# Optimization experiments

Measured on AMD Instinct MI355X. Metric: run time of the kernel, lower is better.

Reference implementation:

```python
import jax, jax.numpy as jnp
import numpy as np
from jax import lax

NEG = -1e30  # safe stand-in for -inf in float32
BLANK = 0


def _ctc_loss(log_probs, targets, logits_lengths, targets_lengths):
    # log_probs: (B, T, V) log-softmax over V; targets: (B, S) with labels in [1, V)
    B, T, V = log_probs.shape
    S = targets.shape[1]
    L = 2 * S + 1

    # extended target sequence with interleaved blanks: [b, t0, b, t1, ..., b]
    ext = jnp.full((B, L), BLANK, dtype=targets.dtype)
    ext = ext.at[:, 1::2].set(targets)

    # skip transition (s-2 -> s) allowed iff ext[s] != blank and ext[s] != ext[s-2]
    shifted2 = jnp.concatenate([jnp.full((B, 2), -1, dtype=ext.dtype), ext[:, :-2]], axis=1)
    skip = (ext != BLANK) & (ext != shifted2)  # (B, L)

    # gather per-time log-probs of extended labels: (B, T, L) -> scan axis first (T, B, L)
    lp_ext = jnp.take_along_axis(log_probs, ext[:, None, :], axis=2)
    xs = jnp.moveaxis(lp_ext, 1, 0)

    alpha0 = jnp.where(jnp.arange(L) == 0, 0.0, NEG).astype(log_probs.dtype)
    alpha0 = jnp.broadcast_to(alpha0, (B, L))

    def step(alpha, inputs):
        lp_t, t = inputs
        a2 = jnp.pad(alpha[:, :-1], ((0, 0), (1, 0)), constant_values=NEG)
        a3 = jnp.pad(alpha[:, :-2], ((0, 0), (2, 0)), constant_values=NEG)
        a3 = jnp.where(skip, a3, NEG)
        new = jnp.logaddexp(jnp.logaddexp(alpha, a2), a3) + lp_t
        # freeze alpha past each sequence's length
        alpha = jnp.where((t < logits_lengths)[:, None], new, alpha)
        return alpha, None

    alpha, _ = lax.scan(step, alpha0, (xs, jnp.arange(T)))

    # final states: last label (2*len-1) and trailing blank (2*len)
    e1 = (2 * targets_lengths - 1)[:, None]
    e2 = (2 * targets_lengths)[:, None]
    l1 = jnp.take_along_axis(alpha, e1, axis=1)[:, 0]
    l2 = jnp.take_along_axis(alpha, e2, axis=1)[:, 0]
    return -jnp.logaddexp(l1, l2)  # (B,)


def setup_inputs() -> dict:
    key = jax.random.key(0)
    k1, k2, k3, k4 = jax.random.split(key, 4)
    B, T, V, S = 64, 2000, 256, 200
    logits = jax.random.normal(k1, (B, T, V), dtype=jnp.float32)
    targets = jax.random.randint(k2, (B, S), 1, V)  # avoid blank=0
    logits_lengths = jax.random.randint(k3, (B,), 1500, T + 1)
    targets_lengths = jax.random.randint(k4, (B,), 150, S + 1)
    return {"logits": logits, "targets": targets,
            "logits_lengths": logits_lengths, "targets_lengths": targets_lengths}


def reference(logits, targets, logits_lengths, targets_lengths):
    # after_logsoftmax=False, time_major=False, reduce=None -> per-sample loss (B,)
    log_probs = jax.nn.log_softmax(logits, axis=2)
    return _ctc_loss(log_probs, targets, logits_lengths, targets_lengths)
```

## Files before the change

### kernel.cpp

```cpp
#include <hip/hip_runtime.h>
#include <hip/hip_bf16.h>
#include <cstdint>

#define NEG  (-1e30f)
#define VSZ  256
#define TCAP 2048
#define LN2F 0.6931471805599453f

typedef __attribute__((ext_vector_type(2))) float f32x2;

static __device__ __forceinline__ float    uifu(unsigned u) { return __uint_as_float(u); }
static __device__ __forceinline__ unsigned f2bf(float f) {
    unsigned u = __float_as_uint(f);
    return (u + 0x7fffu + ((u >> 16) & 1u)) >> 16;
}

static __device__ __forceinline__ unsigned pkbf(float lo, float hi) {
    unsigned r;
    asm("v_cvt_pk_bf16_f32 %0, %1, %2" : "=v"(r) : "v"(lo), "v"(hi));
    return r;
}

static __device__ __forceinline__ float wave_sum_dpp(float v) {
    v += __int_as_float(__builtin_amdgcn_update_dpp(0, __float_as_int(v), 0x111, 0xf, 0xf, true));
    v += __int_as_float(__builtin_amdgcn_update_dpp(0, __float_as_int(v), 0x112, 0xf, 0xf, true));
    v += __int_as_float(__builtin_amdgcn_update_dpp(0, __float_as_int(v), 0x114, 0xf, 0xf, true));
    v += __int_as_float(__builtin_amdgcn_update_dpp(0, __float_as_int(v), 0x118, 0xf, 0xf, true));
    v += __int_as_float(__builtin_amdgcn_update_dpp(0, __float_as_int(v), 0x142, 0xa, 0xf, true));
    v += __int_as_float(__builtin_amdgcn_update_dpp(0, __float_as_int(v), 0x143, 0xc, 0xf, true));
    return __int_as_float(__builtin_amdgcn_readlane(__float_as_int(v), 63));
}

__global__ __launch_bounds__(256) void prep7(const float* __restrict__ logits,
                                             const int* __restrict__ targets,
                                             unsigned short* __restrict__ po,
                                             float* __restrict__ pbf,
                                             int T, int S) {
    const int b    = blockIdx.y;
    const int lane = threadIdx.x & 63;
    const int wv   = threadIdx.x >> 6;
    const int rt   = blockIdx.x * 4 + wv;
    if (rt >= T) return;
    const size_t row = (size_t)b * T + rt;
    __shared__ float ldse[4][VSZ];

    const float4* p = (const float4*)(logits + row * VSZ);
    float4 x = p[lane];
    float4 e;
    e.x = __expf(x.x); e.y = __expf(x.y); e.z = __expf(x.z); e.w = __expf(x.w);
    ((float4*)&ldse[wv][0])[lane] = e;

    float s  = (e.x + e.y) + (e.z + e.w);
    float tot = wave_sum_dpp(s);
    float rs  = __builtin_amdgcn_rcpf(tot);

    const int* tg = targets + (size_t)b * S;
    const int c0 = 4 * lane;
    uint2 st;
    if ((S & 3) == 0) {
        int4 tgv = *(const int4*)(tg + min(c0, S - 4));
        float g0 = ldse[wv][tgv.x] * rs;
        float g1 = ldse[wv][tgv.y] * rs;
        float g2 = ldse[wv][tgv.z] * rs;
        float g3 = ldse[wv][tgv.w] * rs;
        st.x = pkbf(g0, g1);
        st.y = pkbf(g2, g3);
    } else {
        float g0 = 0.f, g1 = 0.f, g2 = 0.f, g3 = 0.f;
        if (c0     < S) g0 = ldse[wv][tg[c0]]     * rs;
        if (c0 + 1 < S) g1 = ldse[wv][tg[c0 + 1]] * rs;
        if (c0 + 2 < S) g2 = ldse[wv][tg[c0 + 2]] * rs;
        if (c0 + 3 < S) g3 = ldse[wv][tg[c0 + 3]] * rs;
        st.x = pkbf(g0, g1);
        st.y = pkbf(g2, g3);
    }
    ((uint2*)(po + row * VSZ))[lane] = st;
    if (lane == 0) pbf[row] = e.x * rs;
}

typedef __attribute__((address_space(1))) unsigned int g1u_t;
typedef __attribute__((address_space(3))) unsigned int l3u_t;

static __device__ __forceinline__ void dma16(const void* g, void* l) {
    __builtin_amdgcn_global_load_lds((g1u_t*)(uintptr_t)g,
                                     (l3u_t*)(unsigned int)(uintptr_t)l, 16, 0, 0);
}
static __device__ __forceinline__ void dma4(const void* g, void* l) {
    __builtin_amdgcn_global_load_lds((g1u_t*)(uintptr_t)g,
                                     (l3u_t*)(unsigned int)(uintptr_t)l, 4, 0, 0);
}
static __device__ __forceinline__ float dpp_shr1_f(float v) {
    return __int_as_float(__builtin_amdgcn_update_dpp(0, __float_as_int(v), 0x138, 0xf, 0xf, true));
}
static __device__ __forceinline__ float dpp_shl1_f(float v) {
    return __int_as_float(__builtin_amdgcn_update_dpp(0, __float_as_int(v), 0x130, 0xf, 0xf, true));
}
static __device__ __forceinline__ int dpp_shr1_i(int v) {
    return __builtin_amdgcn_update_dpp(0, v, 0x138, 0xf, 0xf, true);
}
static __device__ __forceinline__ int dpp_shl1_i(int v) {
    return __builtin_amdgcn_update_dpp(0, v, 0x130, 0xf, 0xf, true);
}

template<int W>
static __device__ __forceinline__ void scan_dir(const unsigned short* __restrict__ po_b,
                                                const float* __restrict__ pbr,
                                                unsigned short* __restrict__ d0,
                                                unsigned short* __restrict__ d1,
                                                float* __restrict__ p0,
                                                float* __restrict__ p1,
                                                int lenD, int lm1, int i,
                                                float m1, float m3, float m5, float m7, float n7,
                                                float A[8], int& E) {
    const int  lhalf = i & 31;
    const bool hi    = (i >= 32);
    float dscale = 1.f;

    f32x2 P73, P51, E62, E40, M73, M51, N75;
    P73.x = A[7]; P73.y = A[3];
    P51.x = A[5]; P51.y = A[1];
    E62.x = A[6]; E62.y = A[2];
    E40.x = A[4]; E40.y = A[0];
    M73.x = m7;  M73.y = m3;
    M51.x = m5;  M51.y = m1;
    N75.x = n7;  N75.y = m5;

    uint2 ra0, ra1, ra2, ra3, ra4, ra5, ra6, ra7;
    uint2 rb0, rb1, rb2, rb3, rb4, rb5, rb6, rb7;
    float4 qaA, qaB, qbA, qbB;

#define ROWOF(t_) (W ? max(lm1 - (t_), 0) : min((t_), lm1))

#define BODY(XV, PBV) { \
    f32x2 pDB, pCA, pbb; \
    pDB.x = uifu(XV.y & 0xffff0000u); pDB.y = uifu(XV.x & 0xffff0000u); \
    pCA.x = uifu(XV.y << 16);         pCA.y = uifu(XV.x << 16); \
    pbb.x = (PBV);                    pbb.y = (PBV); \
    if (W == 0) { \
        float hs = dpp_shr1_f(P73.x) * dscale; \
        f32x2 a3h; a3h.x = P73.y; a3h.y = hs; \
        f32x2 t73 = (__builtin_elementwise_fma(M73, P51, E62) + P73) * pDB; \
        f32x2 t51 = (__builtin_elementwise_fma(M51, a3h, E40) + P51) * pCA; \
        f32x2 t62 = (E62 + P51) * pbb; \
        f32x2 t40 = (E40 + a3h) * pbb; \
        P73 = t73; P51 = t51; E62 = t62; E40 = t40; \
    } else { \
        f32x2 Q73 = P73 * pDB, Q51 = P51 * pCA, Q62 = E62 * pbb, Q40 = E40 * pbb; \
        float nq0 = dpp_shl1_f(Q40.y) * dscale; \
        float nq1 = dpp_shl1_f(Q51.y) * dscale; \
        f32x2 nq04; nq04.x = nq0; nq04.y = Q40.x; \
        f32x2 n1q5; n1q5.x = nq1; n1q5.y = Q51.x; \
        f32x2 t73 = __builtin_elementwise_fma(N75, n1q5, Q73 + nq04); \
        f32x2 t51 = __builtin_elementwise_fma(M73, Q73, Q51 + Q62); \
        f32x2 t62 = Q62 + Q73; \
        f32x2 t40 = Q40 + Q51; \
        P73 = t73; P51 = t51; E62 = t62; E40 = t40; \
    } \
}

#define RENORM { \
    f32x2 mA = __builtin_elementwise_max(__builtin_elementwise_max(P73, P51), \
                                         __builtin_elementwise_max(E62, E40)); \
    float lmx = fmaxf(mA.x, mA.y); \
    unsigned mb = __float_as_uint(lmx) >> 23; \
    mb = mb > 253u ? 253u : mb; \
    float sc_ = uifu((254u - mb) << 23); \
    f32x2 scv; scv.x = sc_; scv.y = sc_; \
    P73 *= scv; P51 *= scv; E62 *= scv; E40 *= scv; \
    E += (int)mb - 127; \
    int he = W ? dpp_shl1_i(E) : dpp_shr1_i(E); \
    int d  = min(max(he - E, -100), 100); \
    dscale = uifu((unsigned)(d + 127) << 23); \
}

#define STAGE(DN, PN_, TBASE) { \
    _Pragma("unroll") \
    for (int u = 0; u < 32; u += 2) { \
        const int rA = ROWOF((TBASE) + u), rB = ROWOF((TBASE) + u + 1); \
        dma16(po_b + (size_t)(hi ? rB : rA) * VSZ + 8 * lhalf, (DN) + (size_t)u * VSZ); \
    } \
    dma4(pbr + ROWOF((TBASE) + lhalf), (PN_)); \
}

#define LDB(R, QA, QB, DC, PC, BASE) { \
    R##0 = *(const uint2*)((DC) + (size_t)((BASE) + 0) * VSZ + 4 * i); \
    R##1 = *(const uint2*)((DC) + (size_t)((BASE) + 1) * VSZ + 4 * i); \
    R##2 = *(const uint2*)((DC) + (size_t)((BASE) + 2) * VSZ + 4 * i); \
    R##3 = *(const uint2*)((DC) + (size_t)((BASE) + 3) * VSZ + 4 * i); \
    R##4 = *(const uint2*)((DC) + (size_t)((BASE) + 4) * VSZ + 4 * i); \
    R##5 = *(const uint2*)((DC) + (size_t)((BASE) + 5) * VSZ + 4 * i); \
    R##6 = *(const uint2*)((DC) + (size_t)((BASE) + 6) * VSZ + 4 * i); \
    R##7 = *(const uint2*)((DC) + (size_t)((BASE) + 7) * VSZ + 4 * i); \
    QA = *(const float4*)((PC) + (BASE)); \
    QB = *(const float4*)((PC) + (BASE) + 4); \
}

#define CMP8(R, QA, QB) { \
    BODY(R##0, QA.x) BODY(R##1, QA.y) BODY(R##2, QA.z) BODY(R##3, QA.w) RENORM \
    BODY(R##4, QB.x) BODY(R##5, QB.y) BODY(R##6, QB.z) BODY(R##7, QB.w) RENORM \
}

#define SBAR __builtin_amdgcn_sched_barrier(0)

#define SUPERF(DC, PC, DN, PN_) { \
    STAGE(DN, PN_, t0 + 32) \
    asm volatile("s_waitcnt vmcnt(17)" ::: "memory"); \
    LDB(ra, qaA, qaB, DC, PC, 0) \
    SBAR; \
    LDB(rb, qbA, qbB, DC, PC, 8) \
    SBAR; \
    CMP8(ra, qaA, qaB) \
    LDB(ra, qaA, qaB, DC, PC, 16) \
    SBAR; \
    CMP8(rb, qbA, qbB) \
    LDB(rb, qbA, qbB, DC, PC, 24) \
    SBAR; \
    CMP8(ra, qaA, qaB) \
    CMP8(rb, qbA, qbB) \
}

    STAGE(d0, p0, 0)

    int t0 = 0;
    const int nfull = lenD >> 5;
    const int ntail = lenD & 31;
    unsigned short* cur = d0; unsigned short* nxt = d1;
    float* pc = p0;  float* pn = p1;

    #pragma clang loop unroll(disable)
    for (int sl = 0; sl < nfull; ++sl) {
        SUPERF(cur, pc, nxt, pn)
        t0 += 32;
        unsigned short* td = cur; cur = nxt; nxt = td;
        float* tp = pc; pc = pn; pn = tp;
    }
    if (ntail) {
        asm volatile("s_waitcnt vmcnt(0)" ::: "memory");
        #pragma clang loop unroll(disable)
        for (int u = 0; u < ntail; ++u) {
            uint2 x = *(const uint2*)(cur + (size_t)u * VSZ + 4 * i);
            float pb = pc[u];
            BODY(x, pb)
            if ((u & 3) == 3) RENORM
        }
    }

    A[7] = P73.x; A[3] = P73.y;
    A[5] = P51.x; A[1] = P51.y;
    A[6] = E62.x; A[2] = E62.y;
    A[4] = E40.x; A[0] = E40.y;
#undef SUPERF
#undef SBAR
#undef CMP8
#undef LDB
#undef STAGE
#undef RENORM
#undef BODY
#undef ROWOF
}

__global__ __launch_bounds__(128, 1) void ctc_scan15(const unsigned short* __restrict__ po,
                                                     const float* __restrict__ pbf,
                                                     const int* __restrict__ targets,
                                                     const int* __restrict__ llen_p,
                                                     const int* __restrict__ tlen_p,
                                                     float* __restrict__ out,
                                                     int T, int S) {
    const int b   = blockIdx.x;
    const int w   = threadIdx.x >> 6;
    const int i   = threadIdx.x & 63;
    const int len  = llen_p[b];
    const int lm1  = len - 1;
    const int lenF = (len + 1) >> 1;
    const int lenD = w ? (len - lenF) : lenF;

    __shared__ __align__(16) unsigned short dF0[32 * VSZ], dF1[32 * VSZ];
    __shared__ __align__(16) unsigned short dB0[32 * VSZ], dB1[32 * VSZ];
    __shared__ __align__(16) float pF0[64], pF1[64], pB0[64], pB1[64];
    __shared__ __align__(16) float bfin[512];
    __shared__ int bein[64];
    __shared__ __align__(16) unsigned char lds_pad[16384];
    if (__builtin_expect(T < 0, 0)) ((volatile unsigned char*)lds_pad)[0] = 1;

    const int* tg  = targets + (size_t)b * S;
    const int Sm1  = S - 1;
    const int j0   = 4 * i;
    const int tm   = tg[max(min(j0 - 1, Sm1), 0)];
    const int t0l  = tg[min(j0,     Sm1)];
    const int t1l  = tg[min(j0 + 1, Sm1)];
    const int t2l  = tg[min(j0 + 2, Sm1)];
    const int t3l  = tg[min(j0 + 3, Sm1)];
    const int t4l  = tg[min(j0 + 4, Sm1)];
    const float m1 = (j0 == 0 || t0l != tm) ? 1.f : 0.f;
    const float m3 = (t1l != t0l) ? 1.f : 0.f;
    const float m5 = (t2l != t1l) ? 1.f : 0.f;
    const float m7 = (t3l != t2l) ? 1.f : 0.f;
    const float n7 = (t4l != t3l) ? 1.f : 0.f;

    const unsigned short* po_b = po + (size_t)b * T * VSZ;
    const float*          pbr  = pbf + (size_t)b * T;

    float A[8];
    int   E = 0;
    if (w == 0) {
        #pragma unroll
        for (int k = 0; k < 8; ++k) A[k] = 0.f;
        if (i == 0) A[0] = 1.f;
        scan_dir<0>(po_b, pbr, dF0, dF1, pF0, pF1,
                    lenD, lm1, i, m1, m3, m5, m7, n7, A, E);
    } else {
        const int tl = tlen_p[b];
        const int s1 = 2 * tl - 1, s2 = 2 * tl;
        #pragma unroll
        for (int k = 0; k < 8; ++k)
            A[k] = (8 * i + k == s1 || 8 * i + k == s2) ? 1.f : 0.f;
        scan_dir<1>(po_b, pbr, dB0, dB1, pB0, pB1,
                    lenD, lm1, i, m1, m3, m5, m7, n7, A, E);
        *(float4*)&bfin[8 * i]     = make_float4(A[0], A[1], A[2], A[3]);
        *(float4*)&bfin[8 * i + 4] = make_float4(A[4], A[5], A[6], A[7]);
        bein[i] = E;
    }
    __syncthreads();
    if (w == 0) {
        float4 u0 = *(float4*)&bfin[8 * i];
        float4 u1 = *(float4*)&bfin[8 * i + 4];
        float dsum = A[0]*u0.x + A[1]*u0.y + A[2]*u0.z + A[3]*u0.w
                   + A[4]*u1.x + A[5]*u1.y + A[6]*u1.z + A[7]*u1.w;
        float li = (dsum > 0.f) ? __logf(dsum) + (float)(E + bein[i]) * LN2F : NEG;
        float mx = li;
        #pragma unroll
        for (int off = 32; off; off >>= 1) mx = fmaxf(mx, __shfl_xor(mx, off, 64));
        float ss = __expf(li - mx);
        #pragma unroll
        for (int off = 32; off; off >>= 1) ss += __shfl_xor(ss, off, 64);
        if (i == 0) out[b] = -(mx + __logf(ss));
    }
}

__device__ __forceinline__ void barrier_lgkm() {
    __asm__ volatile("s_waitcnt lgkmcnt(0)\n\ts_barrier" ::: "memory");
}

__global__ __launch_bounds__(256) void lse_kernel(const float* __restrict__ logits,
                                                  float* __restrict__ lse,
                                                  int nrows) {
    int row = blockIdx.x * 4 + (threadIdx.x >> 6);
    if (row >= nrows) return;
    int lane = threadIdx.x & 63;
    const float4* p = (const float4*)(logits + (size_t)row * VSZ);
    float4 x = p[lane];
    float m = fmaxf(fmaxf(x.x, x.y), fmaxf(x.z, x.w));
    #pragma unroll
    for (int off = 32; off; off >>= 1) m = fmaxf(m, __shfl_xor(m, off, 64));
    float s = __expf(x.x - m) + __expf(x.y - m) + __expf(x.z - m) + __expf(x.w - m);
    #pragma unroll
    for (int off = 32; off; off >>= 1) s += __shfl_xor(s, off, 64);
    if (lane == 0) lse[row] = m + __logf(s);
}

__device__ __forceinline__ float lae(float a, float b) {
    float mx = fmaxf(a, b);
    float mn = fminf(a, b);
    return mx + __logf(1.0f + __expf(mn - mx));
}

__global__ __launch_bounds__(256, 1) void ctc_scan_fb(const float* __restrict__ logits,
                                                      const int* __restrict__ targets,
                                                      const int* __restrict__ llen_p,
                                                      const int* __restrict__ tlen_p,
                                                      const float* __restrict__ lse,
                                                      float* __restrict__ out,
                                                      int T, int S) {
    const int b = blockIdx.x;
    const int i = threadIdx.x;
    const int len = llen_p[b];

    __shared__ float blankv[TCAP];
    __shared__ float abuf[2][256 + 2];
    __shared__ float wsum[4];

    const float* __restrict__ lgb  = logits + (size_t)b * T * VSZ;
    const float* __restrict__ lseb = lse + (size_t)b * T;

    int  lab  = 0;
    bool skip = false;
    if (i < S) {
        lab = targets[b * S + i];
        int prev = (i >= 1) ? targets[b * S + i - 1] : -1;
        skip = (lab != prev);
    }
    for (int t = i; t < len; t += 256) blankv[t] = lgb[(size_t)t * VSZ];
    if (i < 2) abuf[i][0] = NEG;
    __syncthreads();

    float aEven = (i == 0) ? 0.0f : NEG;
    float aOdd  = NEG;
    const int lm1 = len - 1;
    float v0 = lgb[(size_t)lab];
    float v1 = lgb[(size_t)min(1, lm1) * VSZ + lab];
    float v2 = lgb[(size_t)min(2, lm1) * VSZ + lab];

    for (int t = 0; t < len; ++t) {
        float v3 = lgb[(size_t)min(t + 3, lm1) * VSZ + lab];
        float blv = blankv[t];
        abuf[t & 1][i + 1] = aOdd;
        barrier_lgkm();
        float nb = abuf[t & 1][i];
        float ne = lae(aEven, nb) + blv;
        float no = lae(lae(aOdd, aEven), skip ? nb : NEG) + v0;
        aEven = ne; aOdd = no;
        v0 = v1; v1 = v2; v2 = v3;
    }

    blankv[2 * i]     = aEven;
    blankv[2 * i + 1] = aOdd;
    float part = 0.f;
    for (int t = i; t < len; t += 256) part += lseb[t];
    #pragma unroll
    for (int off = 32; off; off >>= 1) part += __shfl_xor(part, off, 64);
    if ((i & 63) == 0) wsum[i >> 6] = part;
    __syncthreads();
    if (i == 0) {
        int tl = tlen_p[b];
        float s = wsum[0] + wsum[1] + wsum[2] + wsum[3];
        out[b] = s - lae(blankv[2 * tl - 1], blankv[2 * tl]);
    }
}

extern "C" void kernel_launch(void* const* d_in, const int* in_sizes, int n_in,
                              void* d_out, int out_size, void* d_ws, size_t ws_size,
                              hipStream_t stream) {
    const float* logits  = (const float*)d_in[0];
    const int*   targets = (const int*)d_in[1];
    const int*   llen    = (const int*)d_in[2];
    const int*   tlen    = (const int*)d_in[3];
    float*       out     = (float*)d_out;

    const int B = in_sizes[2];
    const int S = in_sizes[1] / B;
    const int T = in_sizes[0] / (B * VSZ);
    const int nrows = B * T;

    const size_t need = (size_t)nrows * VSZ * sizeof(unsigned short)
                      + (size_t)nrows * sizeof(float);
    if (ws_size >= need) {
        unsigned short* po = (unsigned short*)d_ws;
        float* pbf = (float*)(po + (size_t)nrows * VSZ);
        dim3 grid((T + 3) / 4, B);
        prep7<<<grid, 256, 0, stream>>>(logits, targets, po, pbf, T, S);
        ctc_scan15<<<B, 128, 0, stream>>>(po, pbf, targets, llen, tlen, out, T, S);
    } else {
        float* lse = (float*)d_ws;
        lse_kernel<<<(nrows + 3) / 4, 256, 0, stream>>>(logits, lse, nrows);
        ctc_scan_fb<<<B, 256, 0, stream>>>(logits, targets, llen, tlen, lse, out, T, S);
    }
}
```

Before: 251.0 us.

## Fuse softmax-gather prep into scan kernel with producer/consumer warp specialization

Removes the separate prep kernel and its bf16 workspace round trip. The scan kernel grows to 256 threads: two producer waves load raw logits into LDS, compute exp and normalize, gather the target probabilities, and write double-buffered bf16 windows. Two consumer waves run the forward and backward scans over those windows, synchronized with block barriers per 32-step window. This trades one launch and a large intermediate write/read for producer compute on the critical path, plus a block-wide barrier per window. With only 64 blocks, most of the GPU sits idle during the exp work.

```diff
diff --git a/kernel.cpp b/kernel.cpp
--- a/kernel.cpp
+++ b/kernel.cpp
@@ -4,16 +4,11 @@
 
 #define NEG  (-1e30f)
 #define VSZ  256
-#define TCAP 2048
 #define LN2F 0.6931471805599453f
 
 typedef __attribute__((ext_vector_type(2))) float f32x2;
 
-static __device__ __forceinline__ float    uifu(unsigned u) { return __uint_as_float(u); }
-static __device__ __forceinline__ unsigned f2bf(float f) {
-    unsigned u = __float_as_uint(f);
-    return (u + 0x7fffu + ((u >> 16) & 1u)) >> 16;
-}
+static __device__ __forceinline__ float uifu(unsigned u) { return __uint_as_float(u); }
 
 static __device__ __forceinline__ unsigned pkbf(float lo, float hi) {
     unsigned r;
@@ -31,53 +26,6 @@
     return __int_as_float(__builtin_amdgcn_readlane(__float_as_int(v), 63));
 }
 
-__global__ __launch_bounds__(256) void prep7(const float* __restrict__ logits,
-                                             const int* __restrict__ targets,
-                                             unsigned short* __restrict__ po,
-                                             float* __restrict__ pbf,
-                                             int T, int S) {
-    const int b    = blockIdx.y;
-    const int lane = threadIdx.x & 63;
-    const int wv   = threadIdx.x >> 6;
-    const int rt   = blockIdx.x * 4 + wv;
-    if (rt >= T) return;
-    const size_t row = (size_t)b * T + rt;
-    __shared__ float ldse[4][VSZ];
-
-    const float4* p = (const float4*)(logits + row * VSZ);
-    float4 x = p[lane];
-    float4 e;
-    e.x = __expf(x.x); e.y = __expf(x.y); e.z = __expf(x.z); e.w = __expf(x.w);
-    ((float4*)&ldse[wv][0])[lane] = e;
-
-    float s  = (e.x + e.y) + (e.z + e.w);
-    float tot = wave_sum_dpp(s);
-    float rs  = __builtin_amdgcn_rcpf(tot);
-
-    const int* tg = targets + (size_t)b * S;
-    const int c0 = 4 * lane;
-    uint2 st;
-    if ((S & 3) == 0) {
-        int4 tgv = *(const int4*)(tg + min(c0, S - 4));
-        float g0 = ldse[wv][tgv.x] * rs;
-        float g1 = ldse[wv][tgv.y] * rs;
-        float g2 = ldse[wv][tgv.z] * rs;
-        float g3 = ldse[wv][tgv.w] * rs;
-        st.x = pkbf(g0, g1);
-        st.y = pkbf(g2, g3);
-    } else {
-        float g0 = 0.f, g1 = 0.f, g2 = 0.f, g3 = 0.f;
-        if (c0     < S) g0 = ldse[wv][tg[c0]]     * rs;
-        if (c0 + 1 < S) g1 = ldse[wv][tg[c0 + 1]] * rs;
-        if (c0 + 2 < S) g2 = ldse[wv][tg[c0 + 2]] * rs;
-        if (c0 + 3 < S) g3 = ldse[wv][tg[c0 + 3]] * rs;
-        st.x = pkbf(g0, g1);
-        st.y = pkbf(g2, g3);
-    }
-    ((uint2*)(po + row * VSZ))[lane] = st;
-    if (lane == 0) pbf[row] = e.x * rs;
-}
-
 typedef __attribute__((address_space(1))) unsigned int g1u_t;
 typedef __attribute__((address_space(3))) unsigned int l3u_t;
 
@@ -85,10 +33,6 @@
     __builtin_amdgcn_global_load_lds((g1u_t*)(uintptr_t)g,
                                      (l3u_t*)(unsigned int)(uintptr_t)l, 16, 0, 0);
 }
-static __device__ __forceinline__ void dma4(const void* g, void* l) {
-    __builtin_amdgcn_global_load_lds((g1u_t*)(uintptr_t)g,
-                                     (l3u_t*)(unsigned int)(uintptr_t)l, 4, 0, 0);
-}
 static __device__ __forceinline__ float dpp_shr1_f(float v) {
     return __int_as_float(__builtin_amdgcn_update_dpp(0, __float_as_int(v), 0x138, 0xf, 0xf, true));
 }
@@ -102,18 +46,70 @@
     return __builtin_amdgcn_update_dpp(0, v, 0x130, 0xf, 0xf, true);
 }
 
+
 template<int W>
-static __device__ __forceinline__ void scan_dir(const unsigned short* __restrict__ po_b,
-                                                const float* __restrict__ pbr,
-                                                unsigned short* __restrict__ d0,
-                                                unsigned short* __restrict__ d1,
-                                                float* __restrict__ p0,
-                                                float* __restrict__ p1,
-                                                int lenD, int lm1, int i,
+static __device__ __forceinline__ void produce_dir(const float* __restrict__ lg_b,
+                                                   int4 tgv,
+                                                   unsigned short* __restrict__ d0,
+                                                   unsigned short* __restrict__ d1,
+                                                   float* __restrict__ p0,
+                                                   float* __restrict__ p1,
+                                                   float* __restrict__ raw,
+                                                   int lenD, int lm1, int i, int nwinMax) {
+#define ROWOF(t_) (W ? max(lm1 - (t_), 0) : min((t_), lm1))
+    const int nwin = (lenD + 31) >> 5;
+
+#define STAGE_RAW(TBASE) { \
+    _Pragma("unroll") \
+    for (int u = 0; u < 32; ++u) \
+        dma16(lg_b + (size_t)ROWOF((TBASE) + u) * VSZ + 4 * i, raw + (size_t)u * VSZ); \
+    asm volatile("s_waitcnt vmcnt(0)" ::: "memory"); \
+}
+
+#define PROCESS(D, P) { \
+    _Pragma("unroll 4") \
+    for (int u = 0; u < 32; ++u) { \
+        float4 x = *(const float4*)(raw + (size_t)u * VSZ + 4 * i); \
+        float4 e; \
+        e.x = __expf(x.x); e.y = __expf(x.y); e.z = __expf(x.z); e.w = __expf(x.w); \
+        *(float4*)(raw + (size_t)u * VSZ + 4 * i) = e; \
+        float s  = (e.x + e.y) + (e.z + e.w); \
+        float rs = __builtin_amdgcn_rcpf(wave_sum_dpp(s)); \
+        float g0 = raw[(size_t)u * VSZ + tgv.x] * rs; \
+        float g1 = raw[(size_t)u * VSZ + tgv.y] * rs; \
+        float g2 = raw[(size_t)u * VSZ + tgv.z] * rs; \
+        float g3 = raw[(size_t)u * VSZ + tgv.w] * rs; \
+        uint2 st; st.x = pkbf(g0, g1); st.y = pkbf(g2, g3); \
+        *(uint2*)((D) + (size_t)u * VSZ + 4 * i) = st; \
+        if (i == 0) (P)[u] = e.x * rs; \
+    } \
+}
+
+    STAGE_RAW(0)
+    PROCESS(d0, p0)
+    #pragma clang loop unroll(disable)
+    for (int k = 0; k < nwinMax; ++k) {
+        __syncthreads();
+        if (k + 1 < nwin) {
+            unsigned short* D = ((k + 1) & 1) ? d1 : d0;
+            float*          P = ((k + 1) & 1) ? p1 : p0;
+            STAGE_RAW(32 * (k + 1))
+            PROCESS(D, P)
+        }
+    }
+#undef PROCESS
+#undef STAGE_RAW
+#undef ROWOF
+}
+
+template<int W>
+static __device__ __forceinline__ void scan_dir(const unsigned short* __restrict__ d0,
+                                                const unsigned short* __restrict__ d1,
+                                                const float* __restrict__ p0,
+                                                const float* __restrict__ p1,
+                                                int lenD, int i,
                                                 float m1, float m3, float m5, float m7, float n7,
-                                                float A[8], int& E) {
-    const int  lhalf = i & 31;
-    const bool hi    = (i >= 32);
+                                                float A[8], int& E, int nwinMax) {
     float dscale = 1.f;
 
     f32x2 P73, P51, E62, E40, M73, M51, N75;
@@ -128,8 +124,6 @@
     uint2 ra0, ra1, ra2, ra3, ra4, ra5, ra6, ra7;
     uint2 rb0, rb1, rb2, rb3, rb4, rb5, rb6, rb7;
     float4 qaA, qaB, qbA, qbB;
-
-#define ROWOF(t_) (W ? max(lm1 - (t_), 0) : min((t_), lm1))
 
 #define BODY(XV, PBV) { \
     f32x2 pDB, pCA, pbb; \
@@ -173,15 +167,6 @@
     dscale = uifu((unsigned)(d + 127) << 23); \
 }
 
-#define STAGE(DN, PN_, TBASE) { \
-    _Pragma("unroll") \
-    for (int u = 0; u < 32; u += 2) { \
-        const int rA = ROWOF((TBASE) + u), rB = ROWOF((TBASE) + u + 1); \
-        dma16(po_b + (size_t)(hi ? rB : rA) * VSZ + 8 * lhalf, (DN) + (size_t)u * VSZ); \
-    } \
-    dma4(pbr + ROWOF((TBASE) + lhalf), (PN_)); \
-}
-
 #define LDB(R, QA, QB, DC, PC, BASE) { \
     R##0 = *(const uint2*)((DC) + (size_t)((BASE) + 0) * VSZ + 4 * i); \
     R##1 = *(const uint2*)((DC) + (size_t)((BASE) + 1) * VSZ + 4 * i); \
@@ -202,46 +187,35 @@
 
 #define SBAR __builtin_amdgcn_sched_barrier(0)
 
-#define SUPERF(DC, PC, DN, PN_) { \
-    STAGE(DN, PN_, t0 + 32) \
-    asm volatile("s_waitcnt vmcnt(17)" ::: "memory"); \
-    LDB(ra, qaA, qaB, DC, PC, 0) \
-    SBAR; \
-    LDB(rb, qbA, qbB, DC, PC, 8) \
-    SBAR; \
-    CMP8(ra, qaA, qaB) \
-    LDB(ra, qaA, qaB, DC, PC, 16) \
-    SBAR; \
-    CMP8(rb, qbA, qbB) \
-    LDB(rb, qbA, qbB, DC, PC, 24) \
-    SBAR; \
-    CMP8(ra, qaA, qaB) \
-    CMP8(rb, qbA, qbB) \
-}
-
-    STAGE(d0, p0, 0)
-
-    int t0 = 0;
     const int nfull = lenD >> 5;
     const int ntail = lenD & 31;
-    unsigned short* cur = d0; unsigned short* nxt = d1;
-    float* pc = p0;  float* pn = p1;
 
     #pragma clang loop unroll(disable)
-    for (int sl = 0; sl < nfull; ++sl) {
-        SUPERF(cur, pc, nxt, pn)
-        t0 += 32;
-        unsigned short* td = cur; cur = nxt; nxt = td;
-        float* tp = pc; pc = pn; pn = tp;
-    }
-    if (ntail) {
-        asm volatile("s_waitcnt vmcnt(0)" ::: "memory");
-        #pragma clang loop unroll(disable)
-        for (int u = 0; u < ntail; ++u) {
-            uint2 x = *(const uint2*)(cur + (size_t)u * VSZ + 4 * i);
-            float pb = pc[u];
-            BODY(x, pb)
-            if ((u & 3) == 3) RENORM
+    for (int k = 0; k < nwinMax; ++k) {
+        __syncthreads();
+        const unsigned short* DC = (k & 1) ? d1 : d0;
+        const float*          PC = (k & 1) ? p1 : p0;
+        if (k < nfull) {
+            LDB(ra, qaA, qaB, DC, PC, 0)
+            SBAR;
+            LDB(rb, qbA, qbB, DC, PC, 8)
+            SBAR;
+            CMP8(ra, qaA, qaB)
+            LDB(ra, qaA, qaB, DC, PC, 16)
+            SBAR;
+            CMP8(rb, qbA, qbB)
+            LDB(rb, qbA, qbB, DC, PC, 24)
+            SBAR;
+            CMP8(ra, qaA, qaB)
+            CMP8(rb, qbA, qbB)
+        } else if (k == nfull && ntail) {
+            #pragma clang loop unroll(disable)
+            for (int u = 0; u < ntail; ++u) {
+                uint2 x = *(const uint2*)(DC + (size_t)u * VSZ + 4 * i);
+                float pb = PC[u];
+                BODY(x, pb)
+                if ((u & 3) == 3) RENORM
+            }
         }
     }
 
@@ -249,18 +223,14 @@
     A[5] = P51.x; A[1] = P51.y;
     A[6] = E62.x; A[2] = E62.y;
     A[4] = E40.x; A[0] = E40.y;
-#undef SUPERF
 #undef SBAR
 #undef CMP8
 #undef LDB
-#undef STAGE
 #undef RENORM
 #undef BODY
-#undef ROWOF
-}
-
-__global__ __launch_bounds__(128, 1) void ctc_scan15(const unsigned short* __restrict__ po,
-                                                     const float* __restrict__ pbf,
+}
+
+__global__ __launch_bounds__(256, 1) void ctc_scan16(const float* __restrict__ logits,
                                                      const int* __restrict__ targets,
                                                      const int* __restrict__ llen_p,
                                                      const int* __restrict__ tlen_p,
@@ -272,50 +242,73 @@
     const int len  = llen_p[b];
     const int lm1  = len - 1;
     const int lenF = (len + 1) >> 1;
-    const int lenD = w ? (len - lenF) : lenF;
+    const int lenB = len - lenF;
+    const int nwinF = (lenF + 31) >> 5;
+    const int nwinB = (lenB + 31) >> 5;
+    const int nwinMax = nwinF > nwinB ? nwinF : nwinB;
 
     __shared__ __align__(16) unsigned short dF0[32 * VSZ], dF1[32 * VSZ];
     __shared__ __align__(16) unsigned short dB0[32 * VSZ], dB1[32 * VSZ];
+    __shared__ __align__(16) float rawF[32 * VSZ];
+    __shared__ __align__(16) float rawB[32 * VSZ];
     __shared__ __align__(16) float pF0[64], pF1[64], pB0[64], pB1[64];
     __shared__ __align__(16) float bfin[512];
     __shared__ int bein[64];
-    __shared__ __align__(16) unsigned char lds_pad[16384];
-    if (__builtin_expect(T < 0, 0)) ((volatile unsigned char*)lds_pad)[0] = 1;
-
-    const int* tg  = targets + (size_t)b * S;
-    const int Sm1  = S - 1;
-    const int j0   = 4 * i;
-    const int tm   = tg[max(min(j0 - 1, Sm1), 0)];
-    const int t0l  = tg[min(j0,     Sm1)];
-    const int t1l  = tg[min(j0 + 1, Sm1)];
-    const int t2l  = tg[min(j0 + 2, Sm1)];
-    const int t3l  = tg[min(j0 + 3, Sm1)];
-    const int t4l  = tg[min(j0 + 4, Sm1)];
-    const float m1 = (j0 == 0 || t0l != tm) ? 1.f : 0.f;
-    const float m3 = (t1l != t0l) ? 1.f : 0.f;
-    const float m5 = (t2l != t1l) ? 1.f : 0.f;
-    const float m7 = (t3l != t2l) ? 1.f : 0.f;
-    const float n7 = (t4l != t3l) ? 1.f : 0.f;
-
-    const unsigned short* po_b = po + (size_t)b * T * VSZ;
-    const float*          pbr  = pbf + (size_t)b * T;
+
+    const float* lg_b = logits + (size_t)b * T * VSZ;
+    const int*   tg   = targets + (size_t)b * S;
+    const int    Sm1  = S - 1;
 
     float A[8];
     int   E = 0;
-    if (w == 0) {
-        #pragma unroll
-        for (int k = 0; k < 8; ++k) A[k] = 0.f;
-        if (i == 0) A[0] = 1.f;
-        scan_dir<0>(po_b, pbr, dF0, dF1, pF0, pF1,
-                    lenD, lm1, i, m1, m3, m5, m7, n7, A, E);
+
+    if (w < 2) {
+        const int j0   = 4 * i;
+        const int tm   = tg[max(min(j0 - 1, Sm1), 0)];
+        const int t0l  = tg[min(j0,     Sm1)];
+        const int t1l  = tg[min(j0 + 1, Sm1)];
+        const int t2l  = tg[min(j0 + 2, Sm1)];
+        const int t3l  = tg[min(j0 + 3, Sm1)];
+        const int t4l  = tg[min(j0 + 4, Sm1)];
+        const float m1 = (j0 == 0 || t0l != tm) ? 1.f : 0.f;
+        const float m3 = (t1l != t0l) ? 1.f : 0.f;
+        const float m5 = (t2l != t1l) ? 1.f : 0.f;
+        const float m7 = (t3l != t2l) ? 1.f : 0.f;
+        const float n7 = (t4l != t3l) ? 1.f : 0.f;
+
+        if (w == 0) {
+            #pragma unroll
+            for (int k = 0; k < 8; ++k) A[k] = 0.f;
+            if (i == 0) A[0] = 1.f;
+            scan_dir<0>(dF0, dF1, pF0, pF1, lenF, i,
+                        m1, m3, m5, m7, n7, A, E, nwinMax);
+        } else {
+            const int tl = tlen_p[b];
+            const int s1 = 2 * tl - 1, s2 = 2 * tl;
+            #pragma unroll
+            for (int k = 0; k < 8; ++k)
+                A[k] = (8 * i + k == s1 || 8 * i + k == s2) ? 1.f : 0.f;
+            scan_dir<1>(dB0, dB1, pB0, pB1, lenB, i,
+                        m1, m3, m5, m7, n7, A, E, nwinMax);
+        }
     } else {
-        const int tl = tlen_p[b];
-        const int s1 = 2 * tl - 1, s2 = 2 * tl;
-        #pragma unroll
-        for (int k = 0; k < 8; ++k)
-            A[k] = (8 * i + k == s1 || 8 * i + k == s2) ? 1.f : 0.f;
-        scan_dir<1>(po_b, pbr, dB0, dB1, pB0, pB1,
-                    lenD, lm1, i, m1, m3, m5, m7, n7, A, E);
+        int4 tgv;
+        if ((S & 3) == 0) {
+            tgv = *(const int4*)(tg + min(4 * i, S - 4));
+        } else {
+            tgv.x = tg[min(4 * i,     Sm1)];
+            tgv.y = tg[min(4 * i + 1, Sm1)];
+            tgv.z = tg[min(4 * i + 2, Sm1)];
+            tgv.w = tg[min(4 * i + 3, Sm1)];
+        }
+        if (w == 2) {
+            produce_dir<0>(lg_b, tgv, dF0, dF1, pF0, pF1, rawF, lenF, lm1, i, nwinMax);
+        } else {
+            produce_dir<1>(lg_b, tgv, dB0, dB1, pB0, pB1, rawB, lenB, lm1, i, nwinMax);
+        }
+    }
+
+    if (w == 1) {
         *(float4*)&bfin[8 * i]     = make_float4(A[0], A[1], A[2], A[3]);
         *(float4*)&bfin[8 * i + 4] = make_float4(A[4], A[5], A[6], A[7]);
         bein[i] = E;
@@ -337,96 +330,6 @@
     }
 }
 
-__device__ __forceinline__ void barrier_lgkm() {
-    __asm__ volatile("s_waitcnt lgkmcnt(0)\n\ts_barrier" ::: "memory");
-}
-
-__global__ __launch_bounds__(256) void lse_kernel(const float* __restrict__ logits,
-                                                  float* __restrict__ lse,
-                                                  int nrows) {
-    int row = blockIdx.x * 4 + (threadIdx.x >> 6);
-    if (row >= nrows) return;
-    int lane = threadIdx.x & 63;
-    const float4* p = (const float4*)(logits + (size_t)row * VSZ);
-    float4 x = p[lane];
-    float m = fmaxf(fmaxf(x.x, x.y), fmaxf(x.z, x.w));
-    #pragma unroll
-    for (int off = 32; off; off >>= 1) m = fmaxf(m, __shfl_xor(m, off, 64));
-    float s = __expf(x.x - m) + __expf(x.y - m) + __expf(x.z - m) + __expf(x.w - m);
-    #pragma unroll
-    for (int off = 32; off; off >>= 1) s += __shfl_xor(s, off, 64);
-    if (lane == 0) lse[row] = m + __logf(s);
-}
-
-__device__ __forceinline__ float lae(float a, float b) {
-    float mx = fmaxf(a, b);
-    float mn = fminf(a, b);
-    return mx + __logf(1.0f + __expf(mn - mx));
-}
-
-__global__ __launch_bounds__(256, 1) void ctc_scan_fb(const float* __restrict__ logits,
-                                                      const int* __restrict__ targets,
-                                                      const int* __restrict__ llen_p,
-                                                      const int* __restrict__ tlen_p,
-                                                      const float* __restrict__ lse,
-                                                      float* __restrict__ out,
-                                                      int T, int S) {
-    const int b = blockIdx.x;
-    const int i = threadIdx.x;
-    const int len = llen_p[b];
-
-    __shared__ float blankv[TCAP];
-    __shared__ float abuf[2][256 + 2];
-    __shared__ float wsum[4];
-
-    const float* __restrict__ lgb  = logits + (size_t)b * T * VSZ;
-    const float* __restrict__ lseb = lse + (size_t)b * T;
-
-    int  lab  = 0;
-    bool skip = false;
-    if (i < S) {
-        lab = targets[b * S + i];
-        int prev = (i >= 1) ? targets[b * S + i - 1] : -1;
-        skip = (lab != prev);
-    }
-    for (int t = i; t < len; t += 256) blankv[t] = lgb[(size_t)t * VSZ];
-    if (i < 2) abuf[i][0] = NEG;
-    __syncthreads();
-
-    float aEven = (i == 0) ? 0.0f : NEG;
-    float aOdd  = NEG;
-    const int lm1 = len - 1;
-    float v0 = lgb[(size_t)lab];
-    float v1 = lgb[(size_t)min(1, lm1) * VSZ + lab];
-    float v2 = lgb[(size_t)min(2, lm1) * VSZ + lab];
-
-    for (int t = 0; t < len; ++t) {
-        float v3 = lgb[(size_t)min(t + 3, lm1) * VSZ + lab];
-        float blv = blankv[t];
-        abuf[t & 1][i + 1] = aOdd;
-        barrier_lgkm();
-        float nb = abuf[t & 1][i];
-        float ne = lae(aEven, nb) + blv;
-        float no = lae(lae(aOdd, aEven), skip ? nb : NEG) + v0;
-        aEven = ne; aOdd = no;
-        v0 = v1; v1 = v2; v2 = v3;
-    }
-
-    blankv[2 * i]     = aEven;
-    blankv[2 * i + 1] = aOdd;
-    float part = 0.f;
-    for (int t = i; t < len; t += 256) part += lseb[t];
-    #pragma unroll
-    for (int off = 32; off; off >>= 1) part += __shfl_xor(part, off, 64);
-    if ((i & 63) == 0) wsum[i >> 6] = part;
-    __syncthreads();
-    if (i == 0) {
-        int tl = tlen_p[b];
-        float s = wsum[0] + wsum[1] + wsum[2] + wsum[3];
-        out[b] = s - lae(blankv[2 * tl - 1], blankv[2 * tl]);
-    }
-}
-
 extern "C" void kernel_launch(void* const* d_in, const int* in_sizes, int n_in,
                               void* d_out, int out_size, void* d_ws, size_t ws_size,
                               hipStream_t stream) {
@@ -439,19 +342,6 @@
     const int B = in_sizes[2];
     const int S = in_sizes[1] / B;
     const int T = in_sizes[0] / (B * VSZ);
-    const int nrows = B * T;
-
-    const size_t need = (size_t)nrows * VSZ * sizeof(unsigned short)
-                      + (size_t)nrows * sizeof(float);
-    if (ws_size >= need) {
-        unsigned short* po = (unsigned short*)d_ws;
-        float* pbf = (float*)(po + (size_t)nrows * VSZ);
-        dim3 grid((T + 3) / 4, B);
-        prep7<<<grid, 256, 0, stream>>>(logits, targets, po, pbf, T, S);
-        ctc_scan15<<<B, 128, 0, stream>>>(po, pbf, targets, llen, tlen, out, T, S);
-    } else {
-        float* lse = (float*)d_ws;
-        lse_kernel<<<(nrows + 3) / 4, 256, 0, stream>>>(logits, lse, nrows);
-        ctc_scan_fb<<<B, 256, 0, stream>>>(logits, targets, llen, tlen, lse, out, T, S);
-    }
-}
+
+    ctc_scan16<<<B, 256, 0, stream>>>(logits, targets, llen, tlen, out, T, S);
+}
```

Measured after the change: 394.2 us. +57.1%, slower.
